# Kernel optimization log

Hardware: AMD Instinct MI355X
Metric: run time of the kernel (lower is better)

## Reference

```python
import jax, jax.numpy as jnp
import numpy as np

D_MODEL = 1024
N_EXPERTS = 4
TOP_K = 32


def setup_inputs() -> dict:
    key = jax.random.key(0)
    k1, k2, k3, k4 = jax.random.split(key, 4)
    b, t, d = 2, 2048, D_MODEL
    n_lts = 8192
    h = jax.random.normal(k1, (b, t, d), dtype=jnp.float32)
    lts = jax.random.normal(k2, (1, n_lts, d), dtype=jnp.float32)
    # router: nn.Linear(d_model, n_experts)
    lim = 1.0 / np.sqrt(d)
    W_router = jax.random.uniform(k3, (N_EXPERTS, d), minval=-lim, maxval=lim, dtype=jnp.float32)
    b_router = jax.random.uniform(k4, (N_EXPERTS,), minval=-lim, maxval=lim, dtype=jnp.float32)
    return {"h": h, "lts": lts, "W_router": W_router, "b_router": b_router}


def reference(h, lts, W_router, b_router):
    b, t, d = h.shape
    n_lts = lts.shape[1]
    top_k = TOP_K
    n_experts = N_EXPERTS

    # router (eval mode: no noise)
    logits = jnp.einsum('btd,ed->bte', h, W_router) + b_router  # (b,t,E)
    expert_weights = jax.nn.softmax(logits, axis=-1)
    expert_idx = jnp.argmax(expert_weights, axis=-1)            # (b,t) int

    entries_per_expert = n_lts // n_experts
    offsets = jnp.minimum(expert_idx * entries_per_expert, n_lts - top_k)  # (b,t)
    indices = offsets[..., None] + jnp.arange(top_k)            # (b,t,k)
    indices = jnp.minimum(indices, n_lts - 1)

    # gather memory slices: lts broadcast over batch -> (b,t,k,d)
    selected = jnp.take(lts[0], indices, axis=0)

    # small attention of each token over its top_k memory entries
    scores = jnp.einsum('btd,btkd->btk', h, selected) / jnp.sqrt(jnp.asarray(d, h.dtype))
    attn = jax.nn.softmax(scores, axis=-1)
    result = jnp.einsum('btk,btkd->btd', attn, selected)
    return result, expert_weights
```

## Files before the change

### kernel.cpp

```cpp
#include <hip/hip_runtime.h>
#include <hip/hip_fp16.h>
#include <math.h>

constexpr int D    = 1024;
constexpr int NEXP = 4;
constexpr int EPP  = 2048;

typedef _Float16 f16x8 __attribute__((ext_vector_type(8)));
typedef float    f32x4 __attribute__((ext_vector_type(4)));

__device__ __forceinline__ unsigned pk2(float a, float b) {
    return __builtin_bit_cast(unsigned, __builtin_amdgcn_cvt_pkrtz(a, b));
}

__global__ __launch_bounds__(256) void prep_kernel(
    const float* __restrict__ lts, _Float16* __restrict__ lts16,
    _Float16* __restrict__ ltsT)
{
    const int e = blockIdx.x >> 4, part = (blockIdx.x >> 2) & 3, dc = blockIdx.x & 3;
    const int tid = threadIdx.x;
    __shared__ __align__(16) _Float16 s[8][256];

    const float4* src = reinterpret_cast<const float4*>(lts);
    #pragma unroll
    for (int i = 0; i < 2; ++i) {
        const int f = tid + 256 * i;
        const int r = f >> 6, c4 = f & 63;
        const float4 v = src[(size_t)(e * EPP + part * 8 + r) * 256 + dc * 64 + c4];
        *reinterpret_cast<uint2*>(&s[r][c4 * 4]) = make_uint2(pk2(v.x, v.y), pk2(v.z, v.w));
    }
    __syncthreads();

    {
        const int r = tid >> 5, c = tid & 31;
        *reinterpret_cast<uint4*>(lts16 + (size_t)(e * 32 + part * 8 + r) * D + dc * 256 + c * 8) =
            *reinterpret_cast<const uint4*>(&s[r][c * 8]);
    }
    {
        _Float16 tmp[8];
        #pragma unroll
        for (int k = 0; k < 8; ++k) tmp[k] = s[k][tid];
        *reinterpret_cast<uint4*>(ltsT + ((size_t)e << 15) + (size_t)(dc * 256 + tid) * 32 + part * 8) =
            *reinterpret_cast<const uint4*>(tmp);
    }
}

__global__ __launch_bounds__(256) void router_kernel(
    const float* __restrict__ h, const float* __restrict__ Wr,
    const float* __restrict__ br, float* __restrict__ out_ew,
    int* __restrict__ eidx, _Float16* __restrict__ h16, int ntok)
{
    const int tid = threadIdx.x, wid = tid >> 6, lane = tid & 63;
    const int tok = blockIdx.x * 4 + wid;
    if (tok >= ntok) return;

    const float4* h4 = reinterpret_cast<const float4*>(h);
    const float4* w4 = reinterpret_cast<const float4*>(Wr);

    float4 av[4];
    float acc[NEXP] = {0.f, 0.f, 0.f, 0.f};
    #pragma unroll
    for (int i = 0; i < 4; ++i) {
        av[i] = h4[(size_t)tok * 256 + lane + 64 * i];
        #pragma unroll
        for (int e = 0; e < NEXP; ++e) {
            const float4 w = w4[e * 256 + lane + 64 * i];
            acc[e] += av[i].x * w.x + av[i].y * w.y + av[i].z * w.z + av[i].w * w.w;
        }
    }
    #pragma unroll
    for (int m = 1; m < 64; m <<= 1)
        #pragma unroll
        for (int e = 0; e < NEXP; ++e) acc[e] += __shfl_xor(acc[e], m);

    const float l0 = acc[0] + br[0], l1 = acc[1] + br[1],
                l2 = acc[2] + br[2], l3 = acc[3] + br[3];
    const float lm = fmaxf(fmaxf(l0, l1), fmaxf(l2, l3));
    const float e0 = __expf(l0 - lm), e1 = __expf(l1 - lm),
                e2 = __expf(l2 - lm), e3 = __expf(l3 - lm);
    const float einv = 1.f / (e0 + e1 + e2 + e3);
    if (lane < NEXP) {
        const float ev = (lane == 0) ? e0 : (lane == 1) ? e1 : (lane == 2) ? e2 : e3;
        out_ew[(size_t)tok * NEXP + lane] = ev * einv;
    }
    int bi = 0; float bv = l0;
    if (l1 > bv) { bv = l1; bi = 1; }
    if (l2 > bv) { bv = l2; bi = 2; }
    if (l3 > bv) { bv = l3; bi = 3; }
    if (lane == 0) eidx[tok] = bi;

    #pragma unroll
    for (int i = 0; i < 4; ++i)
        *reinterpret_cast<uint2*>(h16 + (size_t)tok * D + (lane + 64 * i) * 4) =
            make_uint2(pk2(av[i].x, av[i].y), pk2(av[i].z, av[i].w));
}

__global__ __launch_bounds__(256) void qk_kernel(
    const _Float16* __restrict__ h16, const _Float16* __restrict__ lts16,
    const int* __restrict__ eidx, _Float16* __restrict__ P32,
    int ntok, int chunks)
{
    const int e = blockIdx.x / chunks;
    const int chunk = blockIdx.x - e * chunks;
    const int base = chunk * 16;

    const int tid = threadIdx.x, wid = tid >> 6, lane = tid & 63;
    __shared__ int eix[16];
    __shared__ float S_part[4][16][33];

    if (tid < 16) {
        const int tk = base + tid;
        eix[tid] = (tk < ntok) ? eidx[tk] : -1;
    }
    __syncthreads();

    const int rA = lane & 15, g4 = lane >> 4;
    int hr = base + rA; if (hr > ntok - 1) hr = ntok - 1;
    const _Float16* ap  = h16  + (size_t)hr * D + g4 * 8;
    const _Float16* b0p = lts16 + (size_t)(e * 32 + rA) * D + g4 * 8;
    const _Float16* b1p = b0p + 16 * D;

    f32x4 s0 = {0.f, 0.f, 0.f, 0.f}, s1 = {0.f, 0.f, 0.f, 0.f};
    #pragma unroll
    for (int k = 0; k < 8; ++k) {
        const int kc = wid * 8 + k;
        const f16x8 a  = *reinterpret_cast<const f16x8*>(ap + kc * 32);
        const f16x8 b0 = *reinterpret_cast<const f16x8*>(b0p + kc * 32);
        const f16x8 b1 = *reinterpret_cast<const f16x8*>(b1p + kc * 32);
        s0 = __builtin_amdgcn_mfma_f32_16x16x32_f16(a, b0, s0, 0, 0, 0);
        s1 = __builtin_amdgcn_mfma_f32_16x16x32_f16(a, b1, s1, 0, 0, 0);
    }
    #pragma unroll
    for (int r = 0; r < 4; ++r) {
        S_part[wid][g4 * 4 + r][rA]      = s0[r];
        S_part[wid][g4 * 4 + r][rA + 16] = s1[r];
    }
    __syncthreads();

    const int tr = tid >> 4, sl = tid & 15;
    const float v0 = S_part[0][tr][sl] + S_part[1][tr][sl]
                   + S_part[2][tr][sl] + S_part[3][tr][sl];
    const float v1 = S_part[0][tr][sl + 16] + S_part[1][tr][sl + 16]
                   + S_part[2][tr][sl + 16] + S_part[3][tr][sl + 16];
    constexpr float inv32 = 1.f / 32.f;
    float mx = fmaxf(v0, v1);
    #pragma unroll
    for (int m = 1; m < 16; m <<= 1) mx = fmaxf(mx, __shfl_xor(mx, m));
    const float p0 = __expf((v0 - mx) * inv32);
    const float p1 = __expf((v1 - mx) * inv32);
    float sm = p0 + p1;
    #pragma unroll
    for (int m = 1; m < 16; m <<= 1) sm += __shfl_xor(sm, m);
    const float is = 1.f / sm;

    const int tok = base + tr;
    if (tok < ntok && eix[tr] == e) {
        P32[(size_t)tok * 32 + sl]      = (_Float16)(p0 * is);
        P32[(size_t)tok * 32 + sl + 16] = (_Float16)(p1 * is);
    }
}

__global__ __launch_bounds__(256) void pv_kernel(
    const _Float16* __restrict__ P32, const int* __restrict__ eidx,
    const _Float16* __restrict__ ltsT, float* __restrict__ out_res, int ntok)
{
    const int tile = blockIdx.x >> 2, q = blockIdx.x & 3;
    const int tid = threadIdx.x, wid = tid >> 6, lane = tid & 63;
    __shared__ __align__(16) unsigned char p_lds[16 * 256];

    {
        const int r = tid >> 4, c = tid & 15;
        const int tok = tile * 16 + r;
        uint4 v = make_uint4(0, 0, 0, 0);
        if (tok < ntok) {
            const int ex = eidx[tok];
            if ((c >> 2) == ex)
                v = *reinterpret_cast<const uint4*>(P32 + (size_t)tok * 32 + (c & 3) * 8);
        }
        *reinterpret_cast<uint4*>(p_lds + r * 256 + ((c ^ (r & 7)) << 4)) = v;
    }
    __syncthreads();

    const int rA = lane & 15, g4 = lane >> 4;
    f16x8 pa[4];
    #pragma unroll
    for (int kc = 0; kc < 4; ++kc)
        pa[kc] = *reinterpret_cast<const f16x8*>(
            p_lds + rA * 256 + ((((kc << 2) | g4) ^ (rA & 7)) << 4));

    int toks[4];
    #pragma unroll
    for (int r = 0; r < 4; ++r) toks[r] = tile * 16 + g4 * 4 + r;

    #pragma unroll
    for (int i = 0; i < 4; ++i) {
        const int dimc = q * 256 + wid * 64 + i * 16 + rA;
        f32x4 o = {0.f, 0.f, 0.f, 0.f};
        #pragma unroll
        for (int kc = 0; kc < 4; ++kc) {
            const f16x8 bk = *reinterpret_cast<const f16x8*>(
                ltsT + ((size_t)kc << 15) + (size_t)dimc * 32 + g4 * 8);
            o = __builtin_amdgcn_mfma_f32_16x16x32_f16(pa[kc], bk, o, 0, 0, 0);
        }
        #pragma unroll
        for (int r = 0; r < 4; ++r)
            if (toks[r] < ntok) out_res[(size_t)toks[r] * D + dimc] = o[r];
    }
}

extern "C" void kernel_launch(void* const* d_in, const int* in_sizes, int n_in,
                              void* d_out, int out_size, void* d_ws, size_t ws_size,
                              hipStream_t stream) {
    const float* h   = (const float*)d_in[0];
    const float* lts = (const float*)d_in[1];
    const float* Wr  = (const float*)d_in[2];
    const float* br  = (const float*)d_in[3];

    const int ntok = in_sizes[0] / D;
    float* out_res = (float*)d_out;
    float* out_ew  = out_res + (size_t)ntok * D;

    _Float16* lts16 = (_Float16*)d_ws;
    _Float16* ltsT  = lts16 + (size_t)128 * D;
    _Float16* P32   = ltsT + (size_t)NEXP * D * 32;
    int*      eidx  = (int*)(P32 + (size_t)ntok * 32);
    _Float16* h16   = (_Float16*)(eidx + ntok);

    const int chunks = (ntok + 15) / 16;

    prep_kernel<<<64, 256, 0, stream>>>(lts, lts16, ltsT);
    router_kernel<<<(ntok + 3) / 4, 256, 0, stream>>>(h, Wr, br, out_ew, eidx, h16, ntok);
    qk_kernel<<<NEXP * chunks, 256, 0, stream>>>(h16, lts16, eidx, P32, ntok, chunks);
    pv_kernel<<<chunks * 4, 256, 0, stream>>>(P32, eidx, ltsT, out_res, ntok);
}
```

Before: 39.88 us.

## Fuse prep with router and QK with PV into two kernels

Merges the lts conversion into the router kernel as extra blocks, and fuses the QK-softmax and PV stages into one attention kernel handling 8 tokens per block. The attention kernel computes scores against all 4 experts' 32 entries, then picks the token's expert columns for the softmax. This removes two launches and the P32 round trip through global memory. In exchange it does 4x redundant QK MFMA work and leaves half of each 16-row MFMA tile unused, since only 8 tokens fill it.

After: 48.23 us. +20.9%, slower.

```diff
diff --git a/kernel.cpp b/kernel.cpp
--- a/kernel.cpp
+++ b/kernel.cpp
@@ -13,45 +13,46 @@
     return __builtin_bit_cast(unsigned, __builtin_amdgcn_cvt_pkrtz(a, b));
 }
 
-__global__ __launch_bounds__(256) void prep_kernel(
-    const float* __restrict__ lts, _Float16* __restrict__ lts16,
-    _Float16* __restrict__ ltsT)
+__global__ __launch_bounds__(256) void prep_router_kernel(
+    const float* __restrict__ h, const float* __restrict__ lts,
+    const float* __restrict__ Wr, const float* __restrict__ br,
+    float* __restrict__ out_ew, int* __restrict__ eidx,
+    _Float16* __restrict__ h16, _Float16* __restrict__ lts16,
+    _Float16* __restrict__ ltsT, int ntok)
 {
-    const int e = blockIdx.x >> 4, part = (blockIdx.x >> 2) & 3, dc = blockIdx.x & 3;
     const int tid = threadIdx.x;
-    __shared__ __align__(16) _Float16 s[8][256];
-
-    const float4* src = reinterpret_cast<const float4*>(lts);
-    #pragma unroll
-    for (int i = 0; i < 2; ++i) {
-        const int f = tid + 256 * i;
-        const int r = f >> 6, c4 = f & 63;
-        const float4 v = src[(size_t)(e * EPP + part * 8 + r) * 256 + dc * 64 + c4];
-        *reinterpret_cast<uint2*>(&s[r][c4 * 4]) = make_uint2(pk2(v.x, v.y), pk2(v.z, v.w));
-    }
-    __syncthreads();
-
-    {
-        const int r = tid >> 5, c = tid & 31;
-        *reinterpret_cast<uint4*>(lts16 + (size_t)(e * 32 + part * 8 + r) * D + dc * 256 + c * 8) =
-            *reinterpret_cast<const uint4*>(&s[r][c * 8]);
-    }
-    {
-        _Float16 tmp[8];
-        #pragma unroll
-        for (int k = 0; k < 8; ++k) tmp[k] = s[k][tid];
-        *reinterpret_cast<uint4*>(ltsT + ((size_t)e << 15) + (size_t)(dc * 256 + tid) * 32 + part * 8) =
-            *reinterpret_cast<const uint4*>(tmp);
-    }
-}
-
-__global__ __launch_bounds__(256) void router_kernel(
-    const float* __restrict__ h, const float* __restrict__ Wr,
-    const float* __restrict__ br, float* __restrict__ out_ew,
-    int* __restrict__ eidx, _Float16* __restrict__ h16, int ntok)
-{
-    const int tid = threadIdx.x, wid = tid >> 6, lane = tid & 63;
-    const int tok = blockIdx.x * 4 + wid;
+
+    if (blockIdx.x < 64) {
+        const int e = blockIdx.x >> 4, part = (blockIdx.x >> 2) & 3, dc = blockIdx.x & 3;
+        __shared__ __align__(16) _Float16 s[8][256];
+
+        const float4* src = reinterpret_cast<const float4*>(lts);
+        #pragma unroll
+        for (int i = 0; i < 2; ++i) {
+            const int f = tid + 256 * i;
+            const int r = f >> 6, c4 = f & 63;
+            const float4 v = src[(size_t)(e * EPP + part * 8 + r) * 256 + dc * 64 + c4];
+            *reinterpret_cast<uint2*>(&s[r][c4 * 4]) = make_uint2(pk2(v.x, v.y), pk2(v.z, v.w));
+        }
+        __syncthreads();
+
+        {
+            const int r = tid >> 5, c = tid & 31;
+            *reinterpret_cast<uint4*>(lts16 + (size_t)(e * 32 + part * 8 + r) * D + dc * 256 + c * 8) =
+                *reinterpret_cast<const uint4*>(&s[r][c * 8]);
+        }
+        {
+            _Float16 tmp[8];
+            #pragma unroll
+            for (int k = 0; k < 8; ++k) tmp[k] = s[k][tid];
+            *reinterpret_cast<uint4*>(ltsT + ((size_t)e << 15) + (size_t)(dc * 256 + tid) * 32 + part * 8) =
+                *reinterpret_cast<const uint4*>(tmp);
+        }
+        return;
+    }
+
+    const int wid = tid >> 6, lane = tid & 63;
+    const int tok = (blockIdx.x - 64) * 4 + wid;
     if (tok >= ntok) return;
 
     const float4* h4 = reinterpret_cast<const float4*>(h);
@@ -95,106 +96,80 @@
             make_uint2(pk2(av[i].x, av[i].y), pk2(av[i].z, av[i].w));
 }
 
-__global__ __launch_bounds__(256) void qk_kernel(
+__global__ __launch_bounds__(256) void attn_kernel(
     const _Float16* __restrict__ h16, const _Float16* __restrict__ lts16,
-    const int* __restrict__ eidx, _Float16* __restrict__ P32,
-    int ntok, int chunks)
+    const _Float16* __restrict__ ltsT, const int* __restrict__ eidx,
+    float* __restrict__ out_res, int ntok)
 {
-    const int e = blockIdx.x / chunks;
-    const int chunk = blockIdx.x - e * chunks;
-    const int base = chunk * 16;
-
     const int tid = threadIdx.x, wid = tid >> 6, lane = tid & 63;
-    __shared__ int eix[16];
-    __shared__ float S_part[4][16][33];
-
-    if (tid < 16) {
+    const int base = blockIdx.x * 8;
+
+    __shared__ int eix[8];
+    __shared__ float S[4][8][130];
+    __shared__ __align__(16) unsigned char p_lds[8 * 256];
+
+    if (tid < 8) {
         const int tk = base + tid;
-        eix[tid] = (tk < ntok) ? eidx[tk] : -1;
-    }
-    __syncthreads();
+        eix[tid] = (tk < ntok) ? eidx[tk] : 0;
+    }
+    if (tid < 128) *reinterpret_cast<uint4*>(p_lds + tid * 16) = make_uint4(0, 0, 0, 0);
 
     const int rA = lane & 15, g4 = lane >> 4;
-    int hr = base + rA; if (hr > ntok - 1) hr = ntok - 1;
-    const _Float16* ap  = h16  + (size_t)hr * D + g4 * 8;
-    const _Float16* b0p = lts16 + (size_t)(e * 32 + rA) * D + g4 * 8;
-    const _Float16* b1p = b0p + 16 * D;
-
-    f32x4 s0 = {0.f, 0.f, 0.f, 0.f}, s1 = {0.f, 0.f, 0.f, 0.f};
+    const int arow = rA & 7;
+    int htok = base + arow; if (htok > ntok - 1) htok = ntok - 1;
+    const _Float16* ap = h16 + (size_t)htok * D + g4 * 8;
+
+    f32x4 s[8];
+    #pragma unroll
+    for (int ct = 0; ct < 8; ++ct) s[ct] = (f32x4){0.f, 0.f, 0.f, 0.f};
     #pragma unroll
     for (int k = 0; k < 8; ++k) {
         const int kc = wid * 8 + k;
-        const f16x8 a  = *reinterpret_cast<const f16x8*>(ap + kc * 32);
-        const f16x8 b0 = *reinterpret_cast<const f16x8*>(b0p + kc * 32);
-        const f16x8 b1 = *reinterpret_cast<const f16x8*>(b1p + kc * 32);
-        s0 = __builtin_amdgcn_mfma_f32_16x16x32_f16(a, b0, s0, 0, 0, 0);
-        s1 = __builtin_amdgcn_mfma_f32_16x16x32_f16(a, b1, s1, 0, 0, 0);
-    }
-    #pragma unroll
-    for (int r = 0; r < 4; ++r) {
-        S_part[wid][g4 * 4 + r][rA]      = s0[r];
-        S_part[wid][g4 * 4 + r][rA + 16] = s1[r];
-    }
+        const f16x8 a = *reinterpret_cast<const f16x8*>(ap + kc * 32);
+        #pragma unroll
+        for (int ct = 0; ct < 8; ++ct) {
+            const f16x8 b = *reinterpret_cast<const f16x8*>(
+                lts16 + (size_t)(ct * 16 + rA) * D + kc * 32 + g4 * 8);
+            s[ct] = __builtin_amdgcn_mfma_f32_16x16x32_f16(a, b, s[ct], 0, 0, 0);
+        }
+    }
+    #pragma unroll
+    for (int ct = 0; ct < 8; ++ct)
+        #pragma unroll
+        for (int r = 0; r < 4; ++r) {
+            const int tr = g4 * 4 + r;
+            if (tr < 8) S[wid][tr][ct * 16 + rA] = s[ct][r];
+        }
     __syncthreads();
 
-    const int tr = tid >> 4, sl = tid & 15;
-    const float v0 = S_part[0][tr][sl] + S_part[1][tr][sl]
-                   + S_part[2][tr][sl] + S_part[3][tr][sl];
-    const float v1 = S_part[0][tr][sl + 16] + S_part[1][tr][sl + 16]
-                   + S_part[2][tr][sl + 16] + S_part[3][tr][sl + 16];
-    constexpr float inv32 = 1.f / 32.f;
-    float mx = fmaxf(v0, v1);
-    #pragma unroll
-    for (int m = 1; m < 16; m <<= 1) mx = fmaxf(mx, __shfl_xor(mx, m));
-    const float p0 = __expf((v0 - mx) * inv32);
-    const float p1 = __expf((v1 - mx) * inv32);
-    float sm = p0 + p1;
-    #pragma unroll
-    for (int m = 1; m < 16; m <<= 1) sm += __shfl_xor(sm, m);
-    const float is = 1.f / sm;
-
-    const int tok = base + tr;
-    if (tok < ntok && eix[tr] == e) {
-        P32[(size_t)tok * 32 + sl]      = (_Float16)(p0 * is);
-        P32[(size_t)tok * 32 + sl + 16] = (_Float16)(p1 * is);
-    }
-}
-
-__global__ __launch_bounds__(256) void pv_kernel(
-    const _Float16* __restrict__ P32, const int* __restrict__ eidx,
-    const _Float16* __restrict__ ltsT, float* __restrict__ out_res, int ntok)
-{
-    const int tile = blockIdx.x >> 2, q = blockIdx.x & 3;
-    const int tid = threadIdx.x, wid = tid >> 6, lane = tid & 63;
-    __shared__ __align__(16) unsigned char p_lds[16 * 256];
-
     {
-        const int r = tid >> 4, c = tid & 15;
-        const int tok = tile * 16 + r;
-        uint4 v = make_uint4(0, 0, 0, 0);
-        if (tok < ntok) {
-            const int ex = eidx[tok];
-            if ((c >> 2) == ex)
-                v = *reinterpret_cast<const uint4*>(P32 + (size_t)tok * 32 + (c & 3) * 8);
-        }
-        *reinterpret_cast<uint4*>(p_lds + r * 256 + ((c ^ (r & 7)) << 4)) = v;
+        const int tr = tid >> 5, sl = tid & 31;
+        const int col = eix[tr] * 32 + sl;
+        const float v = S[0][tr][col] + S[1][tr][col] + S[2][tr][col] + S[3][tr][col];
+        constexpr float inv32 = 1.f / 32.f;
+        float mx = v;
+        #pragma unroll
+        for (int m = 1; m < 32; m <<= 1) mx = fmaxf(mx, __shfl_xor(mx, m));
+        const float p = __expf((v - mx) * inv32);
+        float sm = p;
+        #pragma unroll
+        for (int m = 1; m < 32; m <<= 1) sm += __shfl_xor(sm, m);
+        const float pn = p / sm;
+        const int g = col >> 3;
+        *reinterpret_cast<_Float16*>(p_lds + tr * 256 + ((g ^ tr) << 4) + (col & 7) * 2) =
+            (_Float16)pn;
     }
     __syncthreads();
 
-    const int rA = lane & 15, g4 = lane >> 4;
     f16x8 pa[4];
     #pragma unroll
     for (int kc = 0; kc < 4; ++kc)
         pa[kc] = *reinterpret_cast<const f16x8*>(
-            p_lds + rA * 256 + ((((kc << 2) | g4) ^ (rA & 7)) << 4));
-
-    int toks[4];
-    #pragma unroll
-    for (int r = 0; r < 4; ++r) toks[r] = tile * 16 + g4 * 4 + r;
-
-    #pragma unroll
-    for (int i = 0; i < 4; ++i) {
-        const int dimc = q * 256 + wid * 64 + i * 16 + rA;
+            p_lds + arow * 256 + ((((kc << 2) | g4) ^ arow) << 4));
+
+    #pragma unroll
+    for (int i = 0; i < 16; ++i) {
+        const int dimc = wid * 256 + i * 16 + rA;
         f32x4 o = {0.f, 0.f, 0.f, 0.f};
         #pragma unroll
         for (int kc = 0; kc < 4; ++kc) {
@@ -203,8 +178,11 @@
             o = __builtin_amdgcn_mfma_f32_16x16x32_f16(pa[kc], bk, o, 0, 0, 0);
         }
         #pragma unroll
-        for (int r = 0; r < 4; ++r)
-            if (toks[r] < ntok) out_res[(size_t)toks[r] * D + dimc] = o[r];
+        for (int r = 0; r < 4; ++r) {
+            const int tr2 = g4 * 4 + r;
+            if (tr2 < 8 && base + tr2 < ntok)
+                out_res[(size_t)(base + tr2) * D + dimc] = o[r];
+        }
     }
 }
 
@@ -222,14 +200,12 @@
 
     _Float16* lts16 = (_Float16*)d_ws;
     _Float16* ltsT  = lts16 + (size_t)128 * D;
-    _Float16* P32   = ltsT + (size_t)NEXP * D * 32;
-    int*      eidx  = (int*)(P32 + (size_t)ntok * 32);
+    int*      eidx  = (int*)(ltsT + (size_t)NEXP * D * 32);
     _Float16* h16   = (_Float16*)(eidx + ntok);
 
-    const int chunks = (ntok + 15) / 16;
-
-    prep_kernel<<<64, 256, 0, stream>>>(lts, lts16, ltsT);
-    router_kernel<<<(ntok + 3) / 4, 256, 0, stream>>>(h, Wr, br, out_ew, eidx, h16, ntok);
-    qk_kernel<<<NEXP * chunks, 256, 0, stream>>>(h16, lts16, eidx, P32, ntok, chunks);
-    pv_kernel<<<chunks * 4, 256, 0, stream>>>(P32, eidx, ltsT, out_res, ntok);
-}
+    const int rblocks = 64 + (ntok + 3) / 4;
+    prep_router_kernel<<<rblocks, 256, 0, stream>>>(h, lts, Wr, br, out_ew, eidx,
+                                                    h16, lts16, ltsT, ntok);
+    attn_kernel<<<(ntok + 7) / 8, 256, 0, stream>>>(h16, lts16, ltsT, eidx,
+                                                    out_res, ntok);
+}
```
